# Optimization experiments

Measured on AMD Instinct MI355X. Metric: run time of the kernel, lower is better.

The kernel has to match this reference:

```python
import jax, jax.numpy as jnp
import numpy as np

N_EXPERTS = 256
NUM_POINTS = 512
BATCH = 256
SHARE_DIM = 200
BASE_DIM = 20
LABEL_LEN = 2


def setup_inputs() -> dict:
    key = jax.random.key(0)
    ks = jax.random.split(key, 12)
    s_pre = 1.0 / np.sqrt(NUM_POINTS)
    s_share = 1.0 / np.sqrt(NUM_POINTS)
    s_b1 = 1.0 / np.sqrt(SHARE_DIM)
    s_b2 = 1.0 / np.sqrt(BASE_DIM)
    return {
        "x": jax.random.normal(ks[0], (BATCH, NUM_POINTS), dtype=jnp.float32),
        "magnification": jax.random.uniform(ks[1], (N_EXPERTS, BATCH), dtype=jnp.float32),
        # 256 frozen per-expert Linear(num_points, num_points)
        "W_pre": jax.random.uniform(ks[2], (N_EXPERTS, NUM_POINTS, NUM_POINTS), jnp.float32, -s_pre, s_pre),
        "b_pre": jax.random.uniform(ks[3], (N_EXPERTS, NUM_POINTS), jnp.float32, -s_pre, s_pre),
        # shared: Linear(num_points, 200) + SELU
        "W_share": jax.random.uniform(ks[4], (NUM_POINTS, SHARE_DIM), jnp.float32, -s_share, s_share),
        "b_share": jax.random.uniform(ks[5], (SHARE_DIM,), jnp.float32, -s_share, s_share),
        # base: Linear(200,20)+SELU, Linear(20,2)+Softmax(dim=1)
        "W1": jax.random.uniform(ks[6], (SHARE_DIM, BASE_DIM), jnp.float32, -s_b1, s_b1),
        "b1": jax.random.uniform(ks[7], (BASE_DIM,), jnp.float32, -s_b1, s_b1),
        "W2": jax.random.uniform(ks[8], (BASE_DIM, LABEL_LEN), jnp.float32, -s_b2, s_b2),
        "b2": jax.random.uniform(ks[9], (LABEL_LEN,), jnp.float32, -s_b2, s_b2),
    }


def reference(x, magnification, W_pre, b_pre, W_share, b_share, W1, b1, W2, b2):
    # Batch all 256 expert evaluations as one grouped computation.
    # temp[e,b,p] = magnification[e,b] * x[b,p]
    temp = magnification[:, :, None] * x[None, :, :]            # [E,B,P]
    # per-expert frozen linear: grouped GEMM
    h = jnp.einsum("ebp,epq->ebq", temp, W_pre) + b_pre[:, None, :]   # [E,B,P]
    # shared Linear + SELU
    h = jax.nn.selu(jnp.einsum("ebp,ps->ebs", h, W_share) + b_share)  # [E,B,200]
    # base head (shared weights, applied per expert)
    h = jax.nn.selu(jnp.einsum("ebs,st->ebt", h, W1) + b1)            # [E,B,20]
    logits = jnp.einsum("ebt,tl->ebl", h, W2) + b2                    # [E,B,2]
    probs = jax.nn.softmax(logits, axis=-1)  # Softmax(dim=1) on each [B,2] block
    # torch.cat along dim 0 over the 256 experts
    return probs.reshape(N_EXPERTS * x.shape[0], LABEL_LEN)
```

## Files before the change

### kernel.cpp

```cpp
#include <hip/hip_runtime.h>
#include <hip/hip_bf16.h>


typedef float  f32x4  __attribute__((ext_vector_type(4)));
typedef __bf16 bf16x8 __attribute__((ext_vector_type(8)));
typedef int    i32x4  __attribute__((ext_vector_type(4)));

#define MFMA16(a, b, c) __builtin_amdgcn_mfma_f32_16x16x32_bf16((a), (b), (c), 0, 0, 0)

static constexpr int NE = 256, NB = 256, NP = 512, NS = 200, NT = 20;

static constexpr int XS_P = 40;
static constexpr int ST_P = 40;
static constexpr int HT_P = 72;
static constexpr int H2_P = 232;

static constexpr int OFF_XS   = 0;
static constexpr int OFF_ST   = 40960;
static constexpr int OFF_HT   = 51200;
static constexpr int OFF_H2   = 0;
static constexpr int OFF_PART = 118784;
static constexpr int SMEM_BYTES = 122880;


__global__ void prep_x(const float* __restrict__ x, __bf16* __restrict__ xb) {
    int i = blockIdx.x * 256 + threadIdx.x;
    xb[i] = (__bf16)x[i];
}

__global__ void prep_ws(const float* __restrict__ Ws, __bf16* __restrict__ wf) {
    int i = blockIdx.x * 256 + threadIdx.x;
    int e8  = i & 7;
    int l   = (i >> 3) & 63;
    int n16 = (i >> 9) % 14;
    int k32 = (i >> 9) / 14;
    int q = k32 * 32 + (l >> 4) * 8 + e8;
    int s = n16 * 16 + (l & 15);
    float v = (s < NS) ? Ws[q * NS + s] : 0.0f;
    wf[i] = (__bf16)v;
}


__global__ __launch_bounds__(512, 2) void fused_experts(
    const float* __restrict__ mag,
    const float* __restrict__ Wpre,
    const float* __restrict__ bpre,
    const float* __restrict__ bshare,
    const float* __restrict__ W1,
    const float* __restrict__ b1,
    const float* __restrict__ W2,
    const float* __restrict__ b2,
    const __bf16* __restrict__ xb,
    const __bf16* __restrict__ wsf,
    float* __restrict__ out)
{
    __shared__ __align__(16) char smem[SMEM_BYTES];
    __bf16* xs = (__bf16*)(smem + OFF_XS);
    __bf16* st = (__bf16*)(smem + OFF_ST);
    __bf16* ht = (__bf16*)(smem + OFF_HT);

    const int e    = blockIdx.x;
    const int tid  = threadIdx.x;
    const int lane = tid & 63;
    const int wid  = tid >> 6;
    const int wr   = wid >> 1;
    const int wc   = wid & 1;
    const int l15  = lane & 15;
    const int lg   = lane >> 4;

    const int sx_b = tid >> 1;
    const int sx_h = tid & 1;
    const int sw_p = tid >> 4;
    const int sw_q = (tid & 15) * 4;

    const float* WpreE = Wpre + (size_t)e * NP * NP;

    f32x4 acc2[4][7];
#pragma unroll
    for (int i = 0; i < 4; i++)
#pragma unroll
        for (int j = 0; j < 7; j++)
            acc2[i][j] = (f32x4){0.f, 0.f, 0.f, 0.f};

    for (int nt = 0; nt < 8; ++nt) {
        f32x4 acc1[4][2];
#pragma unroll
        for (int i = 0; i < 4; i++)
#pragma unroll
            for (int j = 0; j < 2; j++)
                acc1[i][j] = (f32x4){0.f, 0.f, 0.f, 0.f};

        {
            i32x4 rx0 = *(const i32x4*)(xb + sx_b * NP + sx_h * 16);
            i32x4 rx1 = *(const i32x4*)(xb + sx_b * NP + sx_h * 16 + 8);
            f32x4 rw  = *(const f32x4*)(WpreE + (size_t)sw_p * NP + nt * 64 + sw_q);
            *(i32x4*)(xs + sx_b * XS_P + sx_h * 16)     = rx0;
            *(i32x4*)(xs + sx_b * XS_P + sx_h * 16 + 8) = rx1;
#pragma unroll
            for (int ii = 0; ii < 4; ++ii)
                st[(sw_q + ii) * ST_P + sw_p] = (__bf16)rw[ii];
        }
        __syncthreads();

#pragma unroll 2
        for (int k = 0; k < 16; ++k) {
            const int db = k & 1;
            i32x4 nx0, nx1; f32x4 nw;
            if (k < 15) {
                const int k32 = k + 1;
                nx0 = *(const i32x4*)(xb + sx_b * NP + k32 * 32 + sx_h * 16);
                nx1 = *(const i32x4*)(xb + sx_b * NP + k32 * 32 + sx_h * 16 + 8);
                nw  = *(const f32x4*)(WpreE + (size_t)(k32 * 32 + sw_p) * NP + nt * 64 + sw_q);
            }
            bf16x8 af[4], bfr[2];
            const __bf16* xsb = xs + db * (256 * XS_P);
#pragma unroll
            for (int i = 0; i < 4; i++) {
                const int row = wr * 64 + i * 16 + l15;
                af[i] = *(const bf16x8*)(xsb + row * XS_P + lg * 8);
            }
            const __bf16* stb = st + db * (64 * ST_P);
#pragma unroll
            for (int j = 0; j < 2; j++) {
                const int q = wc * 32 + j * 16 + l15;
                bfr[j] = *(const bf16x8*)(stb + q * ST_P + lg * 8);
            }
#pragma unroll
            for (int i = 0; i < 4; i++)
#pragma unroll
                for (int j = 0; j < 2; j++)
                    acc1[i][j] = MFMA16(af[i], bfr[j], acc1[i][j]);

            if (k < 15) {
                const int nb2 = 1 - db;
                *(i32x4*)(xs + nb2 * (256 * XS_P) + sx_b * XS_P + sx_h * 16)     = nx0;
                *(i32x4*)(xs + nb2 * (256 * XS_P) + sx_b * XS_P + sx_h * 16 + 8) = nx1;
                __bf16* stw = st + nb2 * (64 * ST_P);
#pragma unroll
                for (int ii = 0; ii < 4; ++ii)
                    stw[(sw_q + ii) * ST_P + sw_p] = (__bf16)nw[ii];
            }
            __syncthreads();
        }

#pragma unroll
        for (int j = 0; j < 2; j++) {
            const int qg = nt * 64 + wc * 32 + j * 16 + l15;
            const float bp = bpre[e * NP + qg];
#pragma unroll
            for (int i = 0; i < 4; i++) {
                const int b0 = wr * 64 + i * 16 + lg * 4;
#pragma unroll
                for (int r = 0; r < 4; r++) {
                    const float m = mag[e * NB + b0 + r];
                    const float h = m * acc1[i][j][r] + bp;
                    ht[(b0 + r) * HT_P + wc * 32 + j * 16 + l15] = (__bf16)h;
                }
            }
        }
        __syncthreads();

#pragma unroll
        for (int kk = 0; kk < 2; ++kk) {
            const int k32g = nt * 2 + kk;
            bf16x8 b2f[7], a2[4];
#pragma unroll
            for (int j2 = 0; j2 < 7; j2++) {
                const int n16 = wc * 7 + j2;
                b2f[j2] = *(const bf16x8*)(wsf + (size_t)((k32g * 14 + n16) * 64 + lane) * 8);
            }
#pragma unroll
            for (int i = 0; i < 4; i++) {
                const int row = wr * 64 + i * 16 + l15;
                a2[i] = *(const bf16x8*)(ht + row * HT_P + kk * 32 + lg * 8);
            }
#pragma unroll
            for (int i = 0; i < 4; i++)
#pragma unroll
                for (int j2 = 0; j2 < 7; j2++)
                    acc2[i][j2] = MFMA16(a2[i], b2f[j2], acc2[i][j2]);
        }
        __syncthreads();
    }

    __bf16* h2  = (__bf16*)(smem + OFF_H2);
    float* part = (float*)(smem + OFF_PART);
    const float SC = 1.0507009873554805f;
    const float AL = 1.6732632423543772f;

#pragma unroll
    for (int j2 = 0; j2 < 7; j2++) {
        const int s = wc * 112 + j2 * 16 + l15;
        const float bs = (s < NS) ? bshare[s] : 0.0f;
#pragma unroll
        for (int i = 0; i < 4; i++) {
            const int b0 = wr * 64 + i * 16 + lg * 4;
#pragma unroll
            for (int r = 0; r < 4; r++) {
                float z = acc2[i][j2][r] + bs;
                z = (z > 0.f) ? SC * z : SC * AL * (__expf(z) - 1.f);
                h2[(b0 + r) * H2_P + s] = (__bf16)z;
            }
        }
    }
    __syncthreads();

    {
        const int b  = tid & 255;
        const int th = tid >> 8;
        float u[10];
#pragma unroll
        for (int j = 0; j < 10; j++) u[j] = b1[th * 10 + j];
        for (int s8 = 0; s8 < NS; s8 += 8) {
            bf16x8 hv = *(const bf16x8*)(h2 + b * H2_P + s8);
#pragma unroll
            for (int so = 0; so < 8; so++) {
                const float v = (float)hv[so];
                const float* w1row = W1 + (s8 + so) * NT + th * 10;
#pragma unroll
                for (int j = 0; j < 10; j++) u[j] = fmaf(v, w1row[j], u[j]);
            }
        }
        float p0 = 0.f, p1 = 0.f;
#pragma unroll
        for (int j = 0; j < 10; j++) {
            float v = u[j];
            v = (v > 0.f) ? SC * v : SC * AL * (__expf(v) - 1.f);
            const int t = th * 10 + j;
            p0 = fmaf(v, W2[t * 2 + 0], p0);
            p1 = fmaf(v, W2[t * 2 + 1], p1);
        }
        part[tid * 2 + 0] = p0;
        part[tid * 2 + 1] = p1;
    }
    __syncthreads();

    if (tid < 256) {
        const int b = tid;
        const float l0 = part[b * 2 + 0] + part[(b + 256) * 2 + 0] + b2[0];
        const float l1 = part[b * 2 + 1] + part[(b + 256) * 2 + 1] + b2[1];
        const float mx  = fmaxf(l0, l1);
        const float ex0 = __expf(l0 - mx), ex1 = __expf(l1 - mx);
        const float inv = 1.0f / (ex0 + ex1);
        out[((size_t)e * NB + b) * 2 + 0] = ex0 * inv;
        out[((size_t)e * NB + b) * 2 + 1] = ex1 * inv;
    }
}


extern "C" void kernel_launch(void* const* d_in, const int* in_sizes, int n_in,
                              void* d_out, int out_size, void* d_ws, size_t ws_size,
                              hipStream_t stream) {
    const float* x      = (const float*)d_in[0];
    const float* mag    = (const float*)d_in[1];
    const float* Wpre   = (const float*)d_in[2];
    const float* bpre   = (const float*)d_in[3];
    const float* Wshare = (const float*)d_in[4];
    const float* bshare = (const float*)d_in[5];
    const float* W1     = (const float*)d_in[6];
    const float* b1     = (const float*)d_in[7];
    const float* W2     = (const float*)d_in[8];
    const float* b2     = (const float*)d_in[9];
    float* out = (float*)d_out;

    __bf16* xb  = (__bf16*)d_ws;
    __bf16* wsf = (__bf16*)((char*)d_ws + 262144);

    prep_x <<<512, 256, 0, stream>>>(x, xb);
    prep_ws<<<448, 256, 0, stream>>>(Wshare, wsf);
    fused_experts<<<256, 512, 0, stream>>>(mag, Wpre, bpre, bshare, W1, b1,
                                           W2, b2, xb, wsf, out);
}
```

Measured before the change: 500.1 us.

## Load x as pre-swizzled MFMA fragments from global and flatten k-loop pipeline

Reformats x on the host-side prep kernel into MFMA fragment order so each wave loads its A operands straight from global/L2 into registers, removing the x shared-memory staging. The per-tile k loops are flattened into a single 128-step software pipeline with register double-buffering (x one step ahead, W_pre two steps ahead), and full __syncthreads are replaced by lgkmcnt waits plus s_barrier. Magnification is hoisted into registers and the W_pre tile is stored transposed with a new pitch. This cuts LDS traffic and barrier stalls, at the cost of more register pressure and repeated global reads of x from every block.

```diff
diff --git a/kernel.cpp b/kernel.cpp
--- a/kernel.cpp
+++ b/kernel.cpp
@@ -4,28 +4,41 @@
 
 typedef float  f32x4  __attribute__((ext_vector_type(4)));
 typedef __bf16 bf16x8 __attribute__((ext_vector_type(8)));
+typedef __bf16 bf16x4 __attribute__((ext_vector_type(4)));
+typedef int    i32x2  __attribute__((ext_vector_type(2)));
 typedef int    i32x4  __attribute__((ext_vector_type(4)));
 
 #define MFMA16(a, b, c) __builtin_amdgcn_mfma_f32_16x16x32_bf16((a), (b), (c), 0, 0, 0)
 
-static constexpr int NE = 256, NB = 256, NP = 512, NS = 200, NT = 20;
-
-static constexpr int XS_P = 40;
-static constexpr int ST_P = 40;
-static constexpr int HT_P = 72;
-static constexpr int H2_P = 232;
-
-static constexpr int OFF_XS   = 0;
-static constexpr int OFF_ST   = 40960;
-static constexpr int OFF_HT   = 51200;
+static constexpr int NB = 256, NP = 512, NS = 200;
+
+static constexpr int ST_PITCH = 72;
+static constexpr int ST_BUF   = 64 * ST_PITCH;
+static constexpr int OFF_ST   = 0;
+static constexpr int OFF_HT   = 9216;
+static constexpr int HT_PITCH = 144;
+static constexpr int H2_P     = 232;
 static constexpr int OFF_H2   = 0;
 static constexpr int OFF_PART = 118784;
 static constexpr int SMEM_BYTES = 122880;
 
-
-__global__ void prep_x(const float* __restrict__ x, __bf16* __restrict__ xb) {
-    int i = blockIdx.x * 256 + threadIdx.x;
-    xb[i] = (__bf16)x[i];
+#define LGKM_BARRIER()                                        \
+    do {                                                      \
+        asm volatile("s_waitcnt lgkmcnt(0)" ::: "memory");    \
+        __builtin_amdgcn_s_barrier();                         \
+    } while (0)
+
+
+__global__ void prep_xf(const float* __restrict__ x, __bf16* __restrict__ xf) {
+    int t   = blockIdx.x * 256 + threadIdx.x;
+    int l   = t & 63;
+    int r16 = (t >> 6) & 15;
+    int k32 = t >> 10;
+    const float* src = x + (r16 * 16 + (l & 15)) * NP + k32 * 32 + (l >> 4) * 8;
+    bf16x8 v;
+#pragma unroll
+    for (int e = 0; e < 8; e++) v[e] = (__bf16)src[e];
+    *(bf16x8*)(xf + (size_t)t * 8) = v;
 }
 
 __global__ void prep_ws(const float* __restrict__ Ws, __bf16* __restrict__ wf) {
@@ -41,6 +54,48 @@
 }
 
 
+#define K_STEP(S, XC, XN, WLD, WUSE)                                          \
+    {                                                                         \
+        const int s1_ = (S) + 1, s2_ = (S) + 2;                               \
+        if (s1_ < 128) {                                                      \
+            const int k1_ = s1_ & 15;                                         \
+            _Pragma("unroll")                                                 \
+            for (int i_ = 0; i_ < 4; i_++)                                    \
+                XN[i_] = *(const bf16x8*)(xfw + k1_ * 8192 + i_ * 512);       \
+        }                                                                     \
+        if (s2_ < 128) {                                                      \
+            const int nt2_ = s2_ >> 4, k2_ = s2_ & 15;                        \
+            _Pragma("unroll")                                                 \
+            for (int i_ = 0; i_ < 4; i_++)                                    \
+                WLD[i_] = WpreE[(size_t)(k2_ * 32 + p0 + i_) * NP + nt2_ * 64 + q]; \
+        }                                                                     \
+        {                                                                     \
+            const char* stb_ = smem + OFF_ST + ((S) & 1) * ST_BUF;            \
+            bf16x8 bf_[2];                                                    \
+            _Pragma("unroll")                                                 \
+            for (int j_ = 0; j_ < 2; j_++) {                                  \
+                const int q_ = wc * 32 + j_ * 16 + l15;                       \
+                union { i32x4 u; bf16x8 b; } cv_;                             \
+                i32x2 lo_ = *(const i32x2*)(stb_ + q_ * ST_PITCH + lg * 16);  \
+                i32x2 hi_ = *(const i32x2*)(stb_ + q_ * ST_PITCH + lg * 16 + 8); \
+                cv_.u = (i32x4){lo_.x, lo_.y, hi_.x, hi_.y};                  \
+                bf_[j_] = cv_.b;                                              \
+            }                                                                 \
+            _Pragma("unroll")                                                 \
+            for (int i_ = 0; i_ < 4; i_++)                                    \
+                _Pragma("unroll")                                             \
+                for (int j_ = 0; j_ < 2; j_++)                                \
+                    acc1[i_][j_] = MFMA16(XC[i_], bf_[j_], acc1[i_][j_]);     \
+        }                                                                     \
+        if (s1_ < 128) {                                                      \
+            bf16x4 wv_;                                                       \
+            _Pragma("unroll")                                                 \
+            for (int i_ = 0; i_ < 4; i_++) wv_[i_] = (__bf16)WUSE[i_];        \
+            *(bf16x4*)(smem + OFF_ST + (s1_ & 1) * ST_BUF + q * ST_PITCH + p0 * 2) = wv_; \
+        }                                                                     \
+        LGKM_BARRIER();                                                       \
+    }
+
 __global__ __launch_bounds__(512, 2) void fused_experts(
     const float* __restrict__ mag,
     const float* __restrict__ Wpre,
@@ -50,14 +105,11 @@
     const float* __restrict__ b1,
     const float* __restrict__ W2,
     const float* __restrict__ b2,
-    const __bf16* __restrict__ xb,
+    const __bf16* __restrict__ xf,
     const __bf16* __restrict__ wsf,
     float* __restrict__ out)
 {
     __shared__ __align__(16) char smem[SMEM_BYTES];
-    __bf16* xs = (__bf16*)(smem + OFF_XS);
-    __bf16* st = (__bf16*)(smem + OFF_ST);
-    __bf16* ht = (__bf16*)(smem + OFF_HT);
 
     const int e    = blockIdx.x;
     const int tid  = threadIdx.x;
@@ -68,120 +120,99 @@
     const int l15  = lane & 15;
     const int lg   = lane >> 4;
 
-    const int sx_b = tid >> 1;
-    const int sx_h = tid & 1;
-    const int sw_p = tid >> 4;
-    const int sw_q = (tid & 15) * 4;
+    const int q  = tid & 63;
+    const int p0 = (tid >> 6) * 4;
 
     const float* WpreE = Wpre + (size_t)e * NP * NP;
+    const __bf16* xfw  = xf + (wr * 4 * 64 + lane) * 8;
+
+    f32x4 magv[4];
+#pragma unroll
+    for (int i = 0; i < 4; i++)
+        magv[i] = *(const f32x4*)(mag + e * NB + wr * 64 + i * 16 + lg * 4);
 
     f32x4 acc2[4][7];
 #pragma unroll
     for (int i = 0; i < 4; i++)
 #pragma unroll
-        for (int j = 0; j < 7; j++)
-            acc2[i][j] = (f32x4){0.f, 0.f, 0.f, 0.f};
-
-    for (int nt = 0; nt < 8; ++nt) {
-        f32x4 acc1[4][2];
-#pragma unroll
-        for (int i = 0; i < 4; i++)
-#pragma unroll
-            for (int j = 0; j < 2; j++)
-                acc1[i][j] = (f32x4){0.f, 0.f, 0.f, 0.f};
-
-        {
-            i32x4 rx0 = *(const i32x4*)(xb + sx_b * NP + sx_h * 16);
-            i32x4 rx1 = *(const i32x4*)(xb + sx_b * NP + sx_h * 16 + 8);
-            f32x4 rw  = *(const f32x4*)(WpreE + (size_t)sw_p * NP + nt * 64 + sw_q);
-            *(i32x4*)(xs + sx_b * XS_P + sx_h * 16)     = rx0;
-            *(i32x4*)(xs + sx_b * XS_P + sx_h * 16 + 8) = rx1;
-#pragma unroll
-            for (int ii = 0; ii < 4; ++ii)
-                st[(sw_q + ii) * ST_P + sw_p] = (__bf16)rw[ii];
-        }
-        __syncthreads();
-
-#pragma unroll 2
-        for (int k = 0; k < 16; ++k) {
-            const int db = k & 1;
-            i32x4 nx0, nx1; f32x4 nw;
-            if (k < 15) {
-                const int k32 = k + 1;
-                nx0 = *(const i32x4*)(xb + sx_b * NP + k32 * 32 + sx_h * 16);
-                nx1 = *(const i32x4*)(xb + sx_b * NP + k32 * 32 + sx_h * 16 + 8);
-                nw  = *(const f32x4*)(WpreE + (size_t)(k32 * 32 + sw_p) * NP + nt * 64 + sw_q);
-            }
-            bf16x8 af[4], bfr[2];
-            const __bf16* xsb = xs + db * (256 * XS_P);
-#pragma unroll
-            for (int i = 0; i < 4; i++) {
-                const int row = wr * 64 + i * 16 + l15;
-                af[i] = *(const bf16x8*)(xsb + row * XS_P + lg * 8);
-            }
-            const __bf16* stb = st + db * (64 * ST_P);
+        for (int j = 0; j < 7; j++) acc2[i][j] = (f32x4){0.f, 0.f, 0.f, 0.f};
+    f32x4 acc1[4][2];
+#pragma unroll
+    for (int i = 0; i < 4; i++)
+#pragma unroll
+        for (int j = 0; j < 2; j++) acc1[i][j] = (f32x4){0.f, 0.f, 0.f, 0.f};
+
+    bf16x8 XA[4], XB[4];
+    float  WEV[4], WOD[4], WT[4];
+
+#pragma unroll
+    for (int i = 0; i < 4; i++)
+        XA[i] = *(const bf16x8*)(xfw + i * 512);
+#pragma unroll
+    for (int i = 0; i < 4; i++)
+        WT[i]  = WpreE[(size_t)(p0 + i) * NP + q];
+#pragma unroll
+    for (int i = 0; i < 4; i++)
+        WOD[i] = WpreE[(size_t)(32 + p0 + i) * NP + q];
+    {
+        bf16x4 wv;
+#pragma unroll
+        for (int i = 0; i < 4; i++) wv[i] = (__bf16)WT[i];
+        *(bf16x4*)(smem + OFF_ST + q * ST_PITCH + p0 * 2) = wv;
+    }
+    LGKM_BARRIER();
+
+    __bf16* ht = (__bf16*)(smem + OFF_HT);
+
+    for (int ss = 0; ss < 128; ss += 2) {
+        K_STEP(ss,     XA, XB, WEV, WOD);
+        K_STEP(ss + 1, XB, XA, WOD, WEV);
+
+        if ((ss & 15) == 14) {
+            const int nt = ss >> 4;
+
+            const float bp0 = bpre[e * NP + nt * 64 + wc * 32 + l15];
+            const float bp1 = bpre[e * NP + nt * 64 + wc * 32 + 16 + l15];
 #pragma unroll
             for (int j = 0; j < 2; j++) {
-                const int q = wc * 32 + j * 16 + l15;
-                bfr[j] = *(const bf16x8*)(stb + q * ST_P + lg * 8);
-            }
-#pragma unroll
-            for (int i = 0; i < 4; i++)
-#pragma unroll
-                for (int j = 0; j < 2; j++)
-                    acc1[i][j] = MFMA16(af[i], bfr[j], acc1[i][j]);
-
-            if (k < 15) {
-                const int nb2 = 1 - db;
-                *(i32x4*)(xs + nb2 * (256 * XS_P) + sx_b * XS_P + sx_h * 16)     = nx0;
-                *(i32x4*)(xs + nb2 * (256 * XS_P) + sx_b * XS_P + sx_h * 16 + 8) = nx1;
-                __bf16* stw = st + nb2 * (64 * ST_P);
-#pragma unroll
-                for (int ii = 0; ii < 4; ++ii)
-                    stw[(sw_q + ii) * ST_P + sw_p] = (__bf16)nw[ii];
-            }
-            __syncthreads();
-        }
-
-#pragma unroll
-        for (int j = 0; j < 2; j++) {
-            const int qg = nt * 64 + wc * 32 + j * 16 + l15;
-            const float bp = bpre[e * NP + qg];
-#pragma unroll
-            for (int i = 0; i < 4; i++) {
-                const int b0 = wr * 64 + i * 16 + lg * 4;
-#pragma unroll
-                for (int r = 0; r < 4; r++) {
-                    const float m = mag[e * NB + b0 + r];
-                    const float h = m * acc1[i][j][r] + bp;
-                    ht[(b0 + r) * HT_P + wc * 32 + j * 16 + l15] = (__bf16)h;
+                const float bp = j ? bp1 : bp0;
+#pragma unroll
+                for (int i = 0; i < 4; i++) {
+#pragma unroll
+                    for (int r = 0; r < 4; r++) {
+                        const float h = magv[i][r] * acc1[i][j][r] + bp;
+                        ht[(wr * 64 + i * 16 + lg * 4 + r) * 72 + wc * 32 + j * 16 + l15] = (__bf16)h;
+                    }
                 }
             }
+            LGKM_BARRIER();
+
+#pragma unroll
+            for (int kk = 0; kk < 2; kk++) {
+                bf16x8 wfr[7];
+#pragma unroll
+                for (int j2 = 0; j2 < 7; j2++)
+                    wfr[j2] = *(const bf16x8*)(wsf +
+                        (size_t)((((nt * 2 + kk) * 14) + wc * 7 + j2) * 64 + lane) * 8);
+                bf16x8 a2[4];
+#pragma unroll
+                for (int i = 0; i < 4; i++)
+                    a2[i] = *(const bf16x8*)(ht + (wr * 64 + i * 16 + l15) * 72 + kk * 32 + lg * 8);
+#pragma unroll
+                for (int i = 0; i < 4; i++)
+#pragma unroll
+                    for (int j2 = 0; j2 < 7; j2++)
+                        acc2[i][j2] = MFMA16(a2[i], wfr[j2], acc2[i][j2]);
+            }
+
+#pragma unroll
+            for (int i = 0; i < 4; i++)
+#pragma unroll
+                for (int j = 0; j < 2; j++) acc1[i][j] = (f32x4){0.f, 0.f, 0.f, 0.f};
         }
-        __syncthreads();
-
-#pragma unroll
-        for (int kk = 0; kk < 2; ++kk) {
-            const int k32g = nt * 2 + kk;
-            bf16x8 b2f[7], a2[4];
-#pragma unroll
-            for (int j2 = 0; j2 < 7; j2++) {
-                const int n16 = wc * 7 + j2;
-                b2f[j2] = *(const bf16x8*)(wsf + (size_t)((k32g * 14 + n16) * 64 + lane) * 8);
-            }
-#pragma unroll
-            for (int i = 0; i < 4; i++) {
-                const int row = wr * 64 + i * 16 + l15;
-                a2[i] = *(const bf16x8*)(ht + row * HT_P + kk * 32 + lg * 8);
-            }
-#pragma unroll
-            for (int i = 0; i < 4; i++)
-#pragma unroll
-                for (int j2 = 0; j2 < 7; j2++)
-                    acc2[i][j2] = MFMA16(a2[i], b2f[j2], acc2[i][j2]);
-        }
-        __syncthreads();
-    }
+    }
+
+    __syncthreads();
 
     __bf16* h2  = (__bf16*)(smem + OFF_H2);
     float* part = (float*)(smem + OFF_PART);
@@ -216,22 +247,22 @@
 #pragma unroll
             for (int so = 0; so < 8; so++) {
                 const float v = (float)hv[so];
-                const float* w1row = W1 + (s8 + so) * NT + th * 10;
+                const float* w1row = W1 + (s8 + so) * 20 + th * 10;
 #pragma unroll
                 for (int j = 0; j < 10; j++) u[j] = fmaf(v, w1row[j], u[j]);
             }
         }
-        float p0 = 0.f, p1 = 0.f;
+        float pa = 0.f, pb = 0.f;
 #pragma unroll
         for (int j = 0; j < 10; j++) {
             float v = u[j];
             v = (v > 0.f) ? SC * v : SC * AL * (__expf(v) - 1.f);
             const int t = th * 10 + j;
-            p0 = fmaf(v, W2[t * 2 + 0], p0);
-            p1 = fmaf(v, W2[t * 2 + 1], p1);
+            pa = fmaf(v, W2[t * 2 + 0], pa);
+            pb = fmaf(v, W2[t * 2 + 1], pb);
         }
-        part[tid * 2 + 0] = p0;
-        part[tid * 2 + 1] = p1;
+        part[tid * 2 + 0] = pa;
+        part[tid * 2 + 1] = pb;
     }
     __syncthreads();
 
@@ -263,11 +294,11 @@
     const float* b2     = (const float*)d_in[9];
     float* out = (float*)d_out;
 
-    __bf16* xb  = (__bf16*)d_ws;
+    __bf16* xf  = (__bf16*)d_ws;
     __bf16* wsf = (__bf16*)((char*)d_ws + 262144);
 
-    prep_x <<<512, 256, 0, stream>>>(x, xb);
+    prep_xf<<<64, 256, 0, stream>>>(x, xf);
     prep_ws<<<448, 256, 0, stream>>>(Wshare, wsf);
     fused_experts<<<256, 512, 0, stream>>>(mag, Wpre, bpre, bshare, W1, b1,
-                                           W2, b2, xb, wsf, out);
+                                           W2, b2, xf, wsf, out);
 }
```

Result: faster. 483.4 us (-3.3%).
